# Performance work log

Hardware: AMD Instinct MI355X
Metric: run time of the kernel (lower is better)

Reference implementation:

```python
import jax, jax.numpy as jnp
import numpy as np

N, K, A = 4096, 64, 8      # nodes, level-2 paths per node, attrs per l2-neighbor
D = 128                    # embed_dim
NU, NR, NA = 100000, 32, 5000  # user vocab, rating vocab, attribute vocab


def setup_inputs() -> dict:
    key = jax.random.key(0)
    ks = jax.random.split(key, 12)
    s = 0.02
    return dict(
        nodes=jax.random.randint(ks[0], (N,), 0, NU),
        paths_rel=jax.random.randint(ks[1], (N, K, 2), 0, NR),
        paths_nbr=jax.random.randint(ks[2], (N, K), 0, NU),
        attrs=jax.random.randint(ks[3], (N, K, A), 0, NA),
        u2e=jax.random.normal(ks[4], (NU, D), dtype=jnp.float32) * s,
        r2e=jax.random.normal(ks[5], (NR, D), dtype=jnp.float32) * s,
        ua2e=jax.random.normal(ks[6], (NA, D), dtype=jnp.float32) * s,
        W1=jax.random.normal(ks[7], (4 * D, 2 * D), dtype=jnp.float32) * s,
        b1=jnp.zeros((2 * D,), jnp.float32),
        W2=jax.random.normal(ks[8], (2 * D, D), dtype=jnp.float32) * s,
        b2=jnp.zeros((D,), jnp.float32),
        A1=jax.random.normal(ks[9], (2 * D, D), dtype=jnp.float32) * s,
        ab1=jnp.zeros((D,), jnp.float32),
        A2=jax.random.normal(ks[10], (D, D), dtype=jnp.float32) * s,
        ab2=jnp.zeros((D,), jnp.float32),
        A3=jax.random.normal(ks[11], (D, 1), dtype=jnp.float32) * s,
        ab3=jnp.zeros((1,), jnp.float32),
    )


def reference(nodes, paths_rel, paths_nbr, attrs, u2e, r2e, ua2e,
              W1, b1, W2, b2, A1, ab1, A2, ab2, A3, ab3):
    # per-path embedding gathers
    r1 = r2e[paths_rel[..., 0]]           # [N,K,D]
    r2 = r2e[paths_rel[..., 1]]           # [N,K,D]
    ne = u2e[paths_nbr]                   # [N,K,D]
    ae = ua2e[attrs].sum(axis=2)          # [N,K,A,D] -> [N,K,D] (uvAttrEmbedding sum)
    # concat + 2-layer MLP (w_r1, w_r2)
    x = jnp.concatenate([r1, r2, ne, ae], axis=-1)   # [N,K,4D]
    h = jax.nn.relu(x @ W1 + b1)                     # [N,K,2D]
    h = jax.nn.relu(h @ W2 + b2)                     # [N,K,D]
    # attention vs self embedding
    self_e = u2e[nodes]                              # [N,D]
    c = jnp.concatenate(
        [h, jnp.broadcast_to(self_e[:, None, :], h.shape)], axis=-1)  # [N,K,2D]
    a = jax.nn.relu(c @ A1 + ab1)
    a = jax.nn.relu(a @ A2 + ab2)
    logits = (a @ A3 + ab3)[..., 0]                  # [N,K]
    w = jax.nn.softmax(logits, axis=1)
    # attention-weighted reduce over paths
    return jnp.einsum('nk,nkd->nd', w, h)            # [N,D]
```

## Files before the change

### kernel.cpp

```cpp
#include <hip/hip_runtime.h>
#include <hip/hip_bf16.h>

#define NN 4096
#define KK 64
#define AA 8
#define DD 128

#define R1_SIZE   16896
#define XH_STRIDE 264
#define A_STRIDE  136
#define H2_STRIDE 136

typedef __bf16 bf16x8 __attribute__((ext_vector_type(8)));
typedef short  s16x8  __attribute__((ext_vector_type(8)));
typedef float  f32x4  __attribute__((ext_vector_type(4)));

__device__ __forceinline__ short f2bf(float f) {
    unsigned u = __builtin_bit_cast(unsigned, f);
    u += 0x7FFFu + ((u >> 16) & 1u);
    return (short)(u >> 16);
}
__device__ __forceinline__ float bf2f(short s) {
    unsigned u = ((unsigned)(unsigned short)s) << 16;
    return __builtin_bit_cast(float, u);
}
__device__ __forceinline__ void store_bf8(short* dst, float4 a, float4 b) {
    s16x8 v;
    v[0] = f2bf(a.x); v[1] = f2bf(a.y); v[2] = f2bf(a.z); v[3] = f2bf(a.w);
    v[4] = f2bf(b.x); v[5] = f2bf(b.y); v[6] = f2bf(b.z); v[7] = f2bf(b.w);
    *(s16x8*)dst = v;
}

__global__ void pack_all(const float* __restrict__ W1, const float* __restrict__ W2,
                         const float* __restrict__ A1, const float* __restrict__ A2,
                         short* __restrict__ W1p, short* __restrict__ W2p,
                         short* __restrict__ A1p, short* __restrict__ A2p)
{
    int t = blockIdx.x * 256 + threadIdx.x;
    const float* src; short* dst; int Ncols, ksl, idx;
    if (t < 131072)      { src = W1; dst = W1p; Ncols = 256; ksl = 4; idx = t; }
    else if (t < 163840) { src = W2; dst = W2p; Ncols = 128; ksl = 3; idx = t - 131072; }
    else if (t < 180224) { src = A1; dst = A1p; Ncols = 128; ksl = 2; idx = t - 163840; }
    else                 { src = A2; dst = A2p; Ncols = 128; ksl = 2; idx = t - 180224; }
    int j     = idx & 7;
    int lane  = (idx >> 3) & 63;
    int fi    = idx >> 9;
    int kstep = fi & ((1 << ksl) - 1);
    int ntile = fi >> ksl;
    int k  = kstep * 32 + (lane >> 4) * 8 + j;
    int nn = ntile * 16 + (lane & 15);
    dst[idx] = f2bf(src[(size_t)k * Ncols + nn]);
}

__global__ void prep_s1(const int* __restrict__ nodes, const float* __restrict__ u2e,
                        const float* __restrict__ A1, const float* __restrict__ ab1,
                        float* __restrict__ s1g)
{
    __shared__ float row[DD];
    const int n = blockIdx.x, c = threadIdx.x;
    const int node = nodes[n];
    row[c] = u2e[(size_t)node * DD + c];
    __syncthreads();
    float acc = ab1[c];
#pragma unroll 8
    for (int i = 0; i < DD; ++i)
        acc = fmaf(row[i], A1[(size_t)(DD + i) * DD + c], acc);
    s1g[(size_t)n * DD + c] = acc;
}

__launch_bounds__(512, 4)
__global__ void l2agg_mfma(
    const int* __restrict__ paths_rel,
    const int* __restrict__ paths_nbr,
    const int* __restrict__ attrs,
    const float* __restrict__ u2e,
    const float* __restrict__ r2e,
    const float* __restrict__ ua2e,
    const float* __restrict__ b1,
    const float* __restrict__ b2,
    const float* __restrict__ ab2,
    const float* __restrict__ A3,
    const float* __restrict__ ab3,
    const short* __restrict__ W1p,
    const short* __restrict__ W2p,
    const short* __restrict__ A1p,
    const short* __restrict__ A2p,
    const float* __restrict__ s1g,
    float* __restrict__ out)
{
    __shared__ short reg1[R1_SIZE];
    __shared__ short h2s[KK * H2_STRIDE];
    __shared__ int   idx_lds[KK * AA + KK];
    __shared__ float partials[8 * KK];
    __shared__ float wts[KK];

    const int n    = blockIdx.x;
    const int tid  = threadIdx.x;
    const int lane = tid & 63;
    const int wv   = tid >> 6;
    const int mr   = lane & 15;
    const int q    = lane >> 4;

    {
        const int* ab = attrs + (size_t)n * KK * AA;
        __builtin_amdgcn_global_load_lds(
            (const __attribute__((address_space(1))) void*)(ab + wv * 64 + lane),
            (__attribute__((address_space(3))) void*)(idx_lds + wv * 64), 4, 0, 0);
        if (wv == 0) {
            const int* nb = paths_nbr + (size_t)n * KK;
            __builtin_amdgcn_global_load_lds(
                (const __attribute__((address_space(1))) void*)(nb + lane),
                (__attribute__((address_space(3))) void*)(idx_lds + 512), 4, 0, 0);
        }
    }

#pragma unroll
    for (int pass = 0; pass < 2; ++pass) {
        const int p  = pass * 32 + (tid >> 4);
        const int t  = tid & 15;
        const int o  = t * 8;
        const int pk = n * KK + p;
        const int i0 = paths_rel[pk * 2 + 0];
        const int i1 = paths_rel[pk * 2 + 1];
        float4 r1a = *(const float4*)&r2e[(size_t)i0 * DD + o];
        float4 r1b = *(const float4*)&r2e[(size_t)i0 * DD + o + 4];
        float4 r2a = *(const float4*)&r2e[(size_t)i1 * DD + o];
        float4 r2b = *(const float4*)&r2e[(size_t)i1 * DD + o + 4];
        store_bf8(&reg1[p * XH_STRIDE + o], r1a, r1b);
        store_bf8(&reg1[p * XH_STRIDE + 128 + o], r2a, r2b);
    }
    __syncthreads();

    const short* W1b = W1p + wv * 2 * 16 * 512 + lane * 8;
    f32x4 acc1[4][2] = {};
    bf16x8 bfc[2], bfn[2];
#pragma unroll
    for (int nt = 0; nt < 2; ++nt) bfc[nt] = *(const bf16x8*)&W1b[nt * 8192];
#pragma unroll
    for (int ks = 0; ks < 8; ++ks) {
#pragma unroll
        for (int nt = 0; nt < 2; ++nt)
            bfn[nt] = *(const bf16x8*)&W1b[nt * 8192 + (ks + 1) * 512];
        bf16x8 af[4];
#pragma unroll
        for (int mt = 0; mt < 4; ++mt)
            af[mt] = *(const bf16x8*)&reg1[(mt * 16 + mr) * XH_STRIDE + ks * 32 + q * 8];
#pragma unroll
        for (int nt = 0; nt < 2; ++nt)
#pragma unroll
            for (int mt = 0; mt < 4; ++mt)
                acc1[mt][nt] = __builtin_amdgcn_mfma_f32_16x16x32_bf16(af[mt], bfc[nt], acc1[mt][nt], 0, 0, 0);
#pragma unroll
        for (int nt = 0; nt < 2; ++nt) bfc[nt] = bfn[nt];
    }
    __syncthreads();

#pragma unroll
    for (int pass = 0; pass < 2; ++pass) {
        const int p  = pass * 32 + (tid >> 4);
        const int t  = tid & 15;
        const int o  = t * 8;
        const int nb = idx_lds[512 + p];
        float4 nea = *(const float4*)&u2e[(size_t)nb * DD + o];
        float4 neb = *(const float4*)&u2e[(size_t)nb * DD + o + 4];
        float4 aea = make_float4(0.f, 0.f, 0.f, 0.f);
        float4 aeb = make_float4(0.f, 0.f, 0.f, 0.f);
#pragma unroll
        for (int a = 0; a < AA; ++a) {
            const int ai = idx_lds[p * AA + a];
            float4 va = *(const float4*)&ua2e[(size_t)ai * DD + o];
            float4 vb = *(const float4*)&ua2e[(size_t)ai * DD + o + 4];
            aea.x += va.x; aea.y += va.y; aea.z += va.z; aea.w += va.w;
            aeb.x += vb.x; aeb.y += vb.y; aeb.z += vb.z; aeb.w += vb.w;
        }
        store_bf8(&reg1[p * XH_STRIDE + o], nea, neb);
        store_bf8(&reg1[p * XH_STRIDE + 128 + o], aea, aeb);
    }
    __syncthreads();

#pragma unroll
    for (int ks = 8; ks < 16; ++ks) {
        if (ks < 15) {
#pragma unroll
            for (int nt = 0; nt < 2; ++nt)
                bfn[nt] = *(const bf16x8*)&W1b[nt * 8192 + (ks + 1) * 512];
        }
        bf16x8 af[4];
#pragma unroll
        for (int mt = 0; mt < 4; ++mt)
            af[mt] = *(const bf16x8*)&reg1[(mt * 16 + mr) * XH_STRIDE + (ks - 8) * 32 + q * 8];
#pragma unroll
        for (int nt = 0; nt < 2; ++nt)
#pragma unroll
            for (int mt = 0; mt < 4; ++mt)
                acc1[mt][nt] = __builtin_amdgcn_mfma_f32_16x16x32_bf16(af[mt], bfc[nt], acc1[mt][nt], 0, 0, 0);
        if (ks < 15) {
#pragma unroll
            for (int nt = 0; nt < 2; ++nt) bfc[nt] = bfn[nt];
        }
    }

    const short* W2b = W2p + wv * 8 * 512 + lane * 8;
    bf16x8 g2c = *(const bf16x8*)&W2b[0], g2n;
    __syncthreads();

#pragma unroll
    for (int nt = 0; nt < 2; ++nt) {
        const int col = (wv * 2 + nt) * 16 + mr;
        const float bb = b1[col];
#pragma unroll
        for (int mt = 0; mt < 4; ++mt)
#pragma unroll
            for (int r = 0; r < 4; ++r)
                reg1[(mt * 16 + q * 4 + r) * XH_STRIDE + col] =
                    f2bf(fmaxf(acc1[mt][nt][r] + bb, 0.f));
    }
    __syncthreads();

    f32x4 acc2[4] = {};
#pragma unroll
    for (int ks = 0; ks < 8; ++ks) {
        if (ks < 7) g2n = *(const bf16x8*)&W2b[(ks + 1) * 512];
        bf16x8 af[4];
#pragma unroll
        for (int mt = 0; mt < 4; ++mt)
            af[mt] = *(const bf16x8*)&reg1[(mt * 16 + mr) * XH_STRIDE + ks * 32 + q * 8];
#pragma unroll
        for (int mt = 0; mt < 4; ++mt)
            acc2[mt] = __builtin_amdgcn_mfma_f32_16x16x32_bf16(af[mt], g2c, acc2[mt], 0, 0, 0);
        if (ks < 7) g2c = g2n;
    }

    const short* A1b = A1p + wv * 4 * 512 + lane * 8;
    bf16x8 g3f[4];
#pragma unroll
    for (int ks = 0; ks < 4; ++ks) g3f[ks] = *(const bf16x8*)&A1b[ks * 512];
    const float s1v = s1g[(size_t)n * DD + wv * 16 + mr];

    {
        const int col = wv * 16 + mr;
        const float bb = b2[col];
#pragma unroll
        for (int mt = 0; mt < 4; ++mt)
#pragma unroll
            for (int r = 0; r < 4; ++r)
                h2s[(mt * 16 + q * 4 + r) * H2_STRIDE + col] =
                    f2bf(fmaxf(acc2[mt][r] + bb, 0.f));
    }
    __syncthreads();

    {
        f32x4 acc3[4];
#pragma unroll
        for (int mt = 0; mt < 4; ++mt) {
            acc3[mt][0] = s1v; acc3[mt][1] = s1v; acc3[mt][2] = s1v; acc3[mt][3] = s1v;
        }
#pragma unroll
        for (int ks = 0; ks < 4; ++ks) {
            bf16x8 af[4];
#pragma unroll
            for (int mt = 0; mt < 4; ++mt)
                af[mt] = *(const bf16x8*)&h2s[(mt * 16 + mr) * H2_STRIDE + ks * 32 + q * 8];
#pragma unroll
            for (int mt = 0; mt < 4; ++mt)
                acc3[mt] = __builtin_amdgcn_mfma_f32_16x16x32_bf16(af[mt], g3f[ks], acc3[mt], 0, 0, 0);
        }
        const short* A2b = A2p + wv * 4 * 512 + lane * 8;
        bf16x8 g4f[4];
#pragma unroll
        for (int ks = 0; ks < 4; ++ks) g4f[ks] = *(const bf16x8*)&A2b[ks * 512];

        {
            const int col = wv * 16 + mr;
#pragma unroll
            for (int mt = 0; mt < 4; ++mt)
#pragma unroll
                for (int r = 0; r < 4; ++r)
                    reg1[(mt * 16 + q * 4 + r) * A_STRIDE + col] =
                        f2bf(fmaxf(acc3[mt][r], 0.f));
        }
        __syncthreads();

        f32x4 acc4[4];
        {
            const float bv = ab2[wv * 16 + mr];
#pragma unroll
            for (int mt = 0; mt < 4; ++mt) {
                acc4[mt][0] = bv; acc4[mt][1] = bv; acc4[mt][2] = bv; acc4[mt][3] = bv;
            }
        }
#pragma unroll
        for (int ks = 0; ks < 4; ++ks) {
            bf16x8 af[4];
#pragma unroll
            for (int mt = 0; mt < 4; ++mt)
                af[mt] = *(const bf16x8*)&reg1[(mt * 16 + mr) * A_STRIDE + ks * 32 + q * 8];
#pragma unroll
            for (int mt = 0; mt < 4; ++mt)
                acc4[mt] = __builtin_amdgcn_mfma_f32_16x16x32_bf16(af[mt], g4f[ks], acc4[mt], 0, 0, 0);
        }
        const float av = A3[wv * 16 + mr];
        float pl[4][4];
#pragma unroll
        for (int mt = 0; mt < 4; ++mt)
#pragma unroll
            for (int r = 0; r < 4; ++r)
                pl[mt][r] = fmaxf(acc4[mt][r], 0.f) * av;
#pragma unroll
        for (int off = 1; off < 16; off <<= 1)
#pragma unroll
            for (int mt = 0; mt < 4; ++mt)
#pragma unroll
                for (int r = 0; r < 4; ++r)
                    pl[mt][r] += __shfl_xor(pl[mt][r], off, 64);
        if (mr == 0) {
#pragma unroll
            for (int mt = 0; mt < 4; ++mt)
#pragma unroll
                for (int r = 0; r < 4; ++r)
                    partials[wv * KK + mt * 16 + q * 4 + r] = pl[mt][r];
        }
    }
    __syncthreads();

    if (tid < KK) {
        float l = ab3[0];
#pragma unroll
        for (int w = 0; w < 8; ++w) l += partials[w * KK + tid];
        float m = l;
#pragma unroll
        for (int off = 32; off > 0; off >>= 1) m = fmaxf(m, __shfl_xor(m, off, 64));
        float e = expf(l - m);
        float s = e;
#pragma unroll
        for (int off = 32; off > 0; off >>= 1) s += __shfl_xor(s, off, 64);
        wts[tid] = e / s;
    }
    __syncthreads();

    if (tid < DD) {
        float acc = 0.f;
#pragma unroll 8
        for (int k = 0; k < KK; ++k)
            acc = fmaf(wts[k], bf2f(h2s[k * H2_STRIDE + tid]), acc);
        out[(size_t)n * DD + tid] = acc;
    }
}

extern "C" void kernel_launch(void* const* d_in, const int* in_sizes, int n_in,
                              void* d_out, int out_size, void* d_ws, size_t ws_size,
                              hipStream_t stream)
{
    const int*   nodes     = (const int*)d_in[0];
    const int*   paths_rel = (const int*)d_in[1];
    const int*   paths_nbr = (const int*)d_in[2];
    const int*   attrs     = (const int*)d_in[3];
    const float* u2e  = (const float*)d_in[4];
    const float* r2e  = (const float*)d_in[5];
    const float* ua2e = (const float*)d_in[6];
    const float* W1   = (const float*)d_in[7];
    const float* b1   = (const float*)d_in[8];
    const float* W2   = (const float*)d_in[9];
    const float* b2   = (const float*)d_in[10];
    const float* A1   = (const float*)d_in[11];
    const float* ab1  = (const float*)d_in[12];
    const float* A2   = (const float*)d_in[13];
    const float* ab2  = (const float*)d_in[14];
    const float* A3   = (const float*)d_in[15];
    const float* ab3  = (const float*)d_in[16];
    float* out = (float*)d_out;

    short* wsp = (short*)d_ws;
    short* W1p = wsp;
    short* W2p = wsp + 131072;
    short* A1p = wsp + 163840;
    short* A2p = wsp + 180224;
    float* s1g = (float*)((char*)d_ws + 393216);

    hipLaunchKernelGGL(pack_all, dim3(768), dim3(256), 0, stream,
                       W1, W2, A1, A2, W1p, W2p, A1p, A2p);
    hipLaunchKernelGGL(prep_s1, dim3(NN), dim3(DD), 0, stream,
                       nodes, u2e, A1, ab1, s1g);
    hipLaunchKernelGGL(l2agg_mfma, dim3(NN), dim3(512), 0, stream,
                       paths_rel, paths_nbr, attrs, u2e, r2e, ua2e,
                       b1, b2, ab2, A3, ab3,
                       W1p, W2p, A1p, A2p, s1g, out);
}
```

Baseline: 297.6 us.

## Merge prep kernels, alias LDS buffers, use packed bf16 converts, raise occupancy

Merges the weight-packing and self-embedding projection kernels into one launch, which removes a launch and its inter-kernel gap. The main kernel aliases the partials and weights scratch onto the index buffer to cut LDS use, and raises launch_bounds min-blocks from 4 to 6 to allow more resident blocks. Float-to-bf16 conversions now use the packed hardware convert builtin when it is available. The higher occupancy target may force register spills, and the aliasing is only safe if the index buffer is dead before partials are written.

Result: slower. 362.5 us (+21.8%).

```diff
diff --git a/kernel.cpp b/kernel.cpp
--- a/kernel.cpp
+++ b/kernel.cpp
@@ -12,7 +12,7 @@
 #define H2_STRIDE 136
 
 typedef __bf16 bf16x8 __attribute__((ext_vector_type(8)));
-typedef short  s16x8  __attribute__((ext_vector_type(8)));
+typedef __bf16 bf16x2 __attribute__((ext_vector_type(2)));
 typedef float  f32x4  __attribute__((ext_vector_type(4)));
 
 __device__ __forceinline__ short f2bf(float f) {
@@ -24,51 +24,63 @@
     unsigned u = ((unsigned)(unsigned short)s) << 16;
     return __builtin_bit_cast(float, u);
 }
+__device__ __forceinline__ unsigned f2bf2(float a, float b) {
+#if __has_builtin(__builtin_amdgcn_cvt_pk_bf16_f32)
+    bf16x2 r = __builtin_amdgcn_cvt_pk_bf16_f32(a, b);
+    return __builtin_bit_cast(unsigned, r);
+#else
+    return ((unsigned)(unsigned short)f2bf(a)) | (((unsigned)(unsigned short)f2bf(b)) << 16);
+#endif
+}
 __device__ __forceinline__ void store_bf8(short* dst, float4 a, float4 b) {
-    s16x8 v;
-    v[0] = f2bf(a.x); v[1] = f2bf(a.y); v[2] = f2bf(a.z); v[3] = f2bf(a.w);
-    v[4] = f2bf(b.x); v[5] = f2bf(b.y); v[6] = f2bf(b.z); v[7] = f2bf(b.w);
-    *(s16x8*)dst = v;
-}
-
-__global__ void pack_all(const float* __restrict__ W1, const float* __restrict__ W2,
+    uint4 v;
+    v.x = f2bf2(a.x, a.y);
+    v.y = f2bf2(a.z, a.w);
+    v.z = f2bf2(b.x, b.y);
+    v.w = f2bf2(b.z, b.w);
+    *(uint4*)dst = v;
+}
+
+__global__ void prep_all(const float* __restrict__ W1, const float* __restrict__ W2,
                          const float* __restrict__ A1, const float* __restrict__ A2,
+                         const int* __restrict__ nodes, const float* __restrict__ u2e,
+                         const float* __restrict__ ab1,
                          short* __restrict__ W1p, short* __restrict__ W2p,
-                         short* __restrict__ A1p, short* __restrict__ A2p)
+                         short* __restrict__ A1p, short* __restrict__ A2p,
+                         float* __restrict__ s1g)
 {
-    int t = blockIdx.x * 256 + threadIdx.x;
-    const float* src; short* dst; int Ncols, ksl, idx;
-    if (t < 131072)      { src = W1; dst = W1p; Ncols = 256; ksl = 4; idx = t; }
-    else if (t < 163840) { src = W2; dst = W2p; Ncols = 128; ksl = 3; idx = t - 131072; }
-    else if (t < 180224) { src = A1; dst = A1p; Ncols = 128; ksl = 2; idx = t - 163840; }
-    else                 { src = A2; dst = A2p; Ncols = 128; ksl = 2; idx = t - 180224; }
-    int j     = idx & 7;
-    int lane  = (idx >> 3) & 63;
-    int fi    = idx >> 9;
-    int kstep = fi & ((1 << ksl) - 1);
-    int ntile = fi >> ksl;
-    int k  = kstep * 32 + (lane >> 4) * 8 + j;
-    int nn = ntile * 16 + (lane & 15);
-    dst[idx] = f2bf(src[(size_t)k * Ncols + nn]);
-}
-
-__global__ void prep_s1(const int* __restrict__ nodes, const float* __restrict__ u2e,
-                        const float* __restrict__ A1, const float* __restrict__ ab1,
-                        float* __restrict__ s1g)
-{
-    __shared__ float row[DD];
-    const int n = blockIdx.x, c = threadIdx.x;
-    const int node = nodes[n];
-    row[c] = u2e[(size_t)node * DD + c];
-    __syncthreads();
-    float acc = ab1[c];
+    if (blockIdx.x < 768) {
+        int t = blockIdx.x * 256 + threadIdx.x;
+        const float* src; short* dst; int Ncols, ksl, idx;
+        if (t < 131072)      { src = W1; dst = W1p; Ncols = 256; ksl = 4; idx = t; }
+        else if (t < 163840) { src = W2; dst = W2p; Ncols = 128; ksl = 3; idx = t - 131072; }
+        else if (t < 180224) { src = A1; dst = A1p; Ncols = 128; ksl = 2; idx = t - 163840; }
+        else                 { src = A2; dst = A2p; Ncols = 128; ksl = 2; idx = t - 180224; }
+        int j     = idx & 7;
+        int lane  = (idx >> 3) & 63;
+        int fi    = idx >> 9;
+        int kstep = fi & ((1 << ksl) - 1);
+        int ntile = fi >> ksl;
+        int k  = kstep * 32 + (lane >> 4) * 8 + j;
+        int nn = ntile * 16 + (lane & 15);
+        dst[idx] = f2bf(src[(size_t)k * Ncols + nn]);
+    } else {
+        __shared__ float row[2][DD];
+        const int half = threadIdx.x >> 7;
+        const int c    = threadIdx.x & 127;
+        const int n    = (blockIdx.x - 768) * 2 + half;
+        const int node = nodes[n];
+        row[half][c] = u2e[(size_t)node * DD + c];
+        __syncthreads();
+        float acc = ab1[c];
 #pragma unroll 8
-    for (int i = 0; i < DD; ++i)
-        acc = fmaf(row[i], A1[(size_t)(DD + i) * DD + c], acc);
-    s1g[(size_t)n * DD + c] = acc;
-}
-
-__launch_bounds__(512, 4)
+        for (int i = 0; i < DD; ++i)
+            acc = fmaf(row[half][i], A1[(size_t)(DD + i) * DD + c], acc);
+        s1g[(size_t)n * DD + c] = acc;
+    }
+}
+
+__launch_bounds__(512, 6)
 __global__ void l2agg_mfma(
     const int* __restrict__ paths_rel,
     const int* __restrict__ paths_nbr,
@@ -90,9 +102,9 @@
 {
     __shared__ short reg1[R1_SIZE];
     __shared__ short h2s[KK * H2_STRIDE];
-    __shared__ int   idx_lds[KK * AA + KK];
-    __shared__ float partials[8 * KK];
-    __shared__ float wts[KK];
+    __shared__ int idx_u[576];
+    float* partials = (float*)idx_u;
+    float* wts      = (float*)(idx_u + 512);
 
     const int n    = blockIdx.x;
     const int tid  = threadIdx.x;
@@ -105,12 +117,12 @@
         const int* ab = attrs + (size_t)n * KK * AA;
         __builtin_amdgcn_global_load_lds(
             (const __attribute__((address_space(1))) void*)(ab + wv * 64 + lane),
-            (__attribute__((address_space(3))) void*)(idx_lds + wv * 64), 4, 0, 0);
+            (__attribute__((address_space(3))) void*)(idx_u + wv * 64), 4, 0, 0);
         if (wv == 0) {
             const int* nb = paths_nbr + (size_t)n * KK;
             __builtin_amdgcn_global_load_lds(
                 (const __attribute__((address_space(1))) void*)(nb + lane),
-                (__attribute__((address_space(3))) void*)(idx_lds + 512), 4, 0, 0);
+                (__attribute__((address_space(3))) void*)(idx_u + 512), 4, 0, 0);
         }
     }
 
@@ -160,14 +172,14 @@
         const int p  = pass * 32 + (tid >> 4);
         const int t  = tid & 15;
         const int o  = t * 8;
-        const int nb = idx_lds[512 + p];
+        const int nb = idx_u[512 + p];
         float4 nea = *(const float4*)&u2e[(size_t)nb * DD + o];
         float4 neb = *(const float4*)&u2e[(size_t)nb * DD + o + 4];
         float4 aea = make_float4(0.f, 0.f, 0.f, 0.f);
         float4 aeb = make_float4(0.f, 0.f, 0.f, 0.f);
 #pragma unroll
         for (int a = 0; a < AA; ++a) {
-            const int ai = idx_lds[p * AA + a];
+            const int ai = idx_u[p * AA + a];
             float4 va = *(const float4*)&ua2e[(size_t)ai * DD + o];
             float4 vb = *(const float4*)&ua2e[(size_t)ai * DD + o + 4];
             aea.x += va.x; aea.y += va.y; aea.z += va.z; aea.w += va.w;
@@ -211,9 +223,12 @@
 #pragma unroll
         for (int mt = 0; mt < 4; ++mt)
 #pragma unroll
-            for (int r = 0; r < 4; ++r)
-                reg1[(mt * 16 + q * 4 + r) * XH_STRIDE + col] =
-                    f2bf(fmaxf(acc1[mt][nt][r] + bb, 0.f));
+            for (int r = 0; r < 4; r += 2) {
+                unsigned pk2 = f2bf2(fmaxf(acc1[mt][nt][r] + bb, 0.f),
+                                     fmaxf(acc1[mt][nt][r + 1] + bb, 0.f));
+                reg1[(mt * 16 + q * 4 + r)     * XH_STRIDE + col] = (short)pk2;
+                reg1[(mt * 16 + q * 4 + r + 1) * XH_STRIDE + col] = (short)(pk2 >> 16);
+            }
     }
     __syncthreads();
 
@@ -243,9 +258,12 @@
 #pragma unroll
         for (int mt = 0; mt < 4; ++mt)
 #pragma unroll
-            for (int r = 0; r < 4; ++r)
-                h2s[(mt * 16 + q * 4 + r) * H2_STRIDE + col] =
-                    f2bf(fmaxf(acc2[mt][r] + bb, 0.f));
+            for (int r = 0; r < 4; r += 2) {
+                unsigned pk2 = f2bf2(fmaxf(acc2[mt][r] + bb, 0.f),
+                                     fmaxf(acc2[mt][r + 1] + bb, 0.f));
+                h2s[(mt * 16 + q * 4 + r)     * H2_STRIDE + col] = (short)pk2;
+                h2s[(mt * 16 + q * 4 + r + 1) * H2_STRIDE + col] = (short)(pk2 >> 16);
+            }
     }
     __syncthreads();
 
@@ -275,9 +293,12 @@
 #pragma unroll
             for (int mt = 0; mt < 4; ++mt)
 #pragma unroll
-                for (int r = 0; r < 4; ++r)
-                    reg1[(mt * 16 + q * 4 + r) * A_STRIDE + col] =
-                        f2bf(fmaxf(acc3[mt][r], 0.f));
+                for (int r = 0; r < 4; r += 2) {
+                    unsigned pk2 = f2bf2(fmaxf(acc3[mt][r], 0.f),
+                                         fmaxf(acc3[mt][r + 1], 0.f));
+                    reg1[(mt * 16 + q * 4 + r)     * A_STRIDE + col] = (short)pk2;
+                    reg1[(mt * 16 + q * 4 + r + 1) * A_STRIDE + col] = (short)(pk2 >> 16);
+                }
         }
         __syncthreads();
 
@@ -377,10 +398,9 @@
     short* A2p = wsp + 180224;
     float* s1g = (float*)((char*)d_ws + 393216);
 
-    hipLaunchKernelGGL(pack_all, dim3(768), dim3(256), 0, stream,
-                       W1, W2, A1, A2, W1p, W2p, A1p, A2p);
-    hipLaunchKernelGGL(prep_s1, dim3(NN), dim3(DD), 0, stream,
-                       nodes, u2e, A1, ab1, s1g);
+    hipLaunchKernelGGL(prep_all, dim3(768 + 2048), dim3(256), 0, stream,
+                       W1, W2, A1, A2, nodes, u2e, ab1,
+                       W1p, W2p, A1p, A2p, s1g);
     hipLaunchKernelGGL(l2agg_mfma, dim3(NN), dim3(512), 0, stream,
                        paths_rel, paths_nbr, attrs, u2e, r2e, ua2e,
                        b1, b2, ab2, A3, ab3,
```
